# Optimization experiments

Hardware: AMD Instinct MI355X
Metric: run time of the kernel (lower is better)

## Reference

```python
import jax, jax.numpy as jnp
import numpy as np

WS = 8   # window_size
NH = 4   # num_heads
EPS = 1e-5

def _rel_pos_index(ws):
    # Static Swin relative-position index, computed with numpy (constant).
    coords = np.stack(np.meshgrid(np.arange(ws), np.arange(ws), indexing='ij'))  # [2,ws,ws]
    cf = coords.reshape(2, -1)                       # [2, N]
    rel = cf[:, :, None] - cf[:, None, :]            # [2, N, N]
    rel = rel.transpose(1, 2, 0).copy()              # [N, N, 2]
    rel[:, :, 0] += ws - 1
    rel[:, :, 1] += ws - 1
    rel[:, :, 0] *= 2 * ws - 1
    return jnp.asarray(rel.sum(-1))                  # [N, N] int

def setup_inputs() -> dict:
    key = jax.random.key(0)
    ks = jax.random.split(key, 4)
    B, C, H, W = 8, 64, 256, 256
    return {
        'x': jax.random.normal(ks[0], (B, C, H, W), jnp.float32),
        'norm_w': jnp.ones((C,), jnp.float32),
        'norm_b': jnp.zeros((C,), jnp.float32),
        'qkv_w': jax.random.normal(ks[1], (3 * C, C), jnp.float32) * 0.05,
        'proj_w': jax.random.normal(ks[2], (C, C), jnp.float32) * 0.05,
        'attn_scale': jnp.ones((1,), jnp.float32) * 0.2,
        'rpb_table': jax.random.normal(ks[3], ((2 * WS - 1) ** 2, NH), jnp.float32) * 0.02,
    }

def reference(x, norm_w, norm_b, qkv_w, proj_w, attn_scale, rpb_table):
    B, C, H, W = x.shape
    ws, nh = WS, NH
    hd = C // nh
    N = ws * ws
    nwh, nww = H // ws, W // ws  # H,W multiples of ws -> pad branch is a no-op
    # window partition: [B,C,H,W] -> [B*nwh*nww, N, C]
    xw = x.reshape(B, C, nwh, ws, nww, ws).transpose(0, 2, 4, 3, 5, 1).reshape(-1, N, C)
    # LayerNorm over channels
    mu = xw.mean(-1, keepdims=True)
    var = xw.var(-1, keepdims=True)
    xn = (xw - mu) / jnp.sqrt(var + EPS) * norm_w + norm_b
    # qkv projection (torch Linear: y = x @ W.T), split heads
    qkv = (xn @ qkv_w.T).reshape(-1, N, 3, nh, hd).transpose(2, 0, 3, 1, 4)  # [3, Wn, h, N, hd]
    q, k, v = qkv[0], qkv[1], qkv[2]
    attn = jnp.einsum('whnd,whmd->whnm', q, k) * (hd ** -0.5)  # [Wn, h, N, N]
    # gathered relative position bias
    rpi = _rel_pos_index(ws)                      # [N, N]
    bias = rpb_table[rpi].transpose(2, 0, 1)      # [h, N, N]
    attn = jax.nn.softmax(attn + bias[None], axis=-1)
    out = jnp.einsum('whnm,whmd->whnd', attn, v)  # [Wn, h, N, hd]
    out = out.transpose(0, 2, 1, 3).reshape(-1, N, C)
    out = out @ proj_w.T
    # window reverse: -> [B, C, H, W]
    out = out.reshape(B, nwh, nww, ws, ws, C).transpose(0, 5, 1, 3, 2, 4).reshape(B, C, H, W)
    return x + attn_scale * out
```

## Files before the change

### kernel.cpp

```cpp
#include <hip/hip_runtime.h>
#include <hip/hip_bf16.h>

#define WSZ 8
#define NHE 4
#define CH 64

typedef unsigned short u16;
typedef __attribute__((ext_vector_type(8))) short short8;
typedef __attribute__((ext_vector_type(4))) short short4v;
typedef __attribute__((ext_vector_type(4))) float float4v;

__device__ __forceinline__ u16 f2bf(float f) {
    __hip_bfloat16 h = __float2bfloat16(f);
    return __builtin_bit_cast(u16, h);
}
__device__ __forceinline__ int SW(int row, int col) {
    return row * 64 + (col ^ ((row & 7) << 3));
}

#define MFMA(a, b, c) __builtin_amdgcn_mfma_f32_16x16x32_bf16(a, b, c, 0, 0, 0)
#define QKSC 0.36067376022224085f

__global__ void prep(const float* __restrict__ qkvw, const float* __restrict__ projw,
                     const float* __restrict__ rpb,
                     u16* __restrict__ wq, u16* __restrict__ wp, float* __restrict__ bl)
{
    int t = blockIdx.x * 256 + threadIdx.x;
    if (t < 12288) {
        int j = t & 7, nl = (t >> 3) & 15, q = (t >> 7) & 3, kt = (t >> 9) & 1, nt = t >> 10;
        wq[t] = f2bf(qkvw[(nt * 16 + nl) * CH + kt * 32 + q * 8 + j]);
    }
    if (t < 4096) {
        int j = t & 7, nl = (t >> 3) & 15, q = (t >> 7) & 3, kt = (t >> 9) & 1, wv = t >> 10;
        wp[t] = f2bf(projw[(wv * 16 + nl) * CH + kt * 32 + q * 8 + j]);
    }
    if (t < 16384) {
        int r = t & 3, nt = (t >> 2) & 3, lane = (t >> 4) & 63, mt = (t >> 10) & 3, h = t >> 12;
        int nl = lane & 15, q = lane >> 4;
        int tokm = mt * 16 + nl, tokn = nt * 16 + q * 4 + r;
        int im = tokm >> 3, jm = tokm & 7, in_ = tokn >> 3, jn = tokn & 7;
        bl[t] = rpb[((im - in_ + 7) * 15 + (jm - jn + 7)) * NHE + h] * 1.44269504088896341f;
    }
}

__global__ __launch_bounds__(256, 5) void win_attn(
    const float* __restrict__ x, const float* __restrict__ nw, const float* __restrict__ nb,
    const u16* __restrict__ wq, const u16* __restrict__ wp,
    const float* __restrict__ ascale, const float* __restrict__ biasl,
    float* __restrict__ out, int B, int H, int W)
{
    const int HWsz = H * W;
    const int nww = W / WSZ, nwh = H / WSZ;
    const int win = (blockIdx.x & 7) * ((int)gridDim.x >> 3) + (blockIdx.x >> 3);
    const int ww = win % nww;
    const int t1 = win / nww;
    const int wh = t1 % nwh;
    const int b  = t1 / nwh;

    const int tid  = threadIdx.x;
    const int lane = tid & 63;
    const int wv   = tid >> 6;
    const int q    = lane >> 4;
    const int nl   = lane & 15;

    __shared__ alignas(16) char smem[32768];
    u16*   XN  = (u16*)(smem);
    u16*   QW  = (u16*)(smem + 8192) + wv * 3072;
    u16*   KW  = QW + 1024;
    u16*   VW  = QW + 2048;
    float* PS  = (float*)(smem + 8192);
    float* PS2 = PS + 256;

    const int rowbase = (wh * WSZ) * W + ww * WSZ;
    const float* xw = x + (size_t)b * CH * HWsz + rowbase;
    const int tokoff = (lane >> 3) * W + (lane & 7);

    float xv[16];
    {
        const float* xc = xw + (size_t)(wv * 16) * HWsz + tokoff;
        #pragma unroll
        for (int ci = 0; ci < 16; ci++) xv[ci] = xc[(size_t)ci * HWsz];
        float s = 0.f, s2 = 0.f;
        #pragma unroll
        for (int ci = 0; ci < 16; ci++) { s += xv[ci]; s2 += xv[ci] * xv[ci]; }
        PS[wv * 64 + lane] = s;
        PS2[wv * 64 + lane] = s2;
    }
    __syncthreads();

    {
        float s  = PS[lane]  + PS[64 + lane]  + PS[128 + lane]  + PS[192 + lane];
        float s2 = PS2[lane] + PS2[64 + lane] + PS2[128 + lane] + PS2[192 + lane];
        float mu  = s * (1.f / 64.f);
        float var = s2 * (1.f / 64.f) - mu * mu;
        float rs  = rsqrtf(var + 1e-5f);
        float v[16];
        #pragma unroll
        for (int ci = 0; ci < 16; ci++) {
            int c = wv * 16 + ci;
            v[ci] = (xv[ci] - mu) * rs * nw[c] + nb[c];
        }
        #pragma unroll
        for (int g = 0; g < 2; g++) {
            short8 pk;
            #pragma unroll
            for (int j = 0; j < 8; j++) pk[j] = (short)f2bf(v[g * 8 + j]);
            *(short8*)&XN[lane * 64 + ((wv * 16 + g * 8) ^ ((lane & 7) << 3))] = pk;
        }
    }
    __syncthreads();

    short8 afr[4][2];
    #pragma unroll
    for (int mt = 0; mt < 4; mt++)
        #pragma unroll
        for (int kt = 0; kt < 2; kt++) {
            int m = mt * 16 + nl;
            int phys = (kt * 4 + q) ^ (m & 7);
            afr[mt][kt] = *(short8*)&XN[m * 64 + phys * 8];
        }
    short8 bfrs[3][2];
    #pragma unroll
    for (int nt3 = 0; nt3 < 3; nt3++) {
        int nt = wv + nt3 * 4;
        #pragma unroll
        for (int kt = 0; kt < 2; kt++)
            bfrs[nt3][kt] = *(const short8*)&wq[((((nt * 2 + kt) * 4 + q) * 16) + nl) * 8];
    }
    __syncthreads();

    #pragma unroll
    for (int nt3 = 0; nt3 < 3; nt3++) {
        #pragma unroll
        for (int mt = 0; mt < 4; mt++) {
            float4v acc = {0.f, 0.f, 0.f, 0.f};
            acc = MFMA(afr[mt][0], bfrs[nt3][0], acc);
            acc = MFMA(afr[mt][1], bfrs[nt3][1], acc);
            int tok0 = mt * 16 + q * 4;
            if (nt3 == 0) {
                #pragma unroll
                for (int r = 0; r < 4; r++) QW[(tok0 + r) * 16 + nl] = f2bf(acc[r]);
            } else if (nt3 == 1) {
                #pragma unroll
                for (int r = 0; r < 4; r++) KW[(tok0 + r) * 16 + nl] = f2bf(acc[r]);
            } else {
                short4v pk;
                pk[0] = (short)f2bf(acc[0]); pk[1] = (short)f2bf(acc[1]);
                pk[2] = (short)f2bf(acc[2]); pk[3] = (short)f2bf(acc[3]);
                int pt = tok0 ^ ((nl & 7) << 3);
                *(short4v*)&VW[nl * 64 + pt] = pk;
            }
        }
    }

    {
        const int h = wv;
        const short8 zero8 = {0, 0, 0, 0, 0, 0, 0, 0};
        short8 kfr[4], vfr[2];
        #pragma unroll
        for (int nt = 0; nt < 4; nt++)
            kfr[nt] = (q < 2) ? *(short8*)&KW[(nt * 16 + nl) * 16 + q * 8] : zero8;
        #pragma unroll
        for (int kt = 0; kt < 2; kt++) {
            int phys = (kt * 4 + q) ^ (nl & 7);
            vfr[kt] = *(short8*)&VW[nl * 64 + phys * 8];
        }
        u16* Pw = KW;
        #pragma unroll
        for (int mt = 0; mt < 4; mt++) {
            short8 qf = (q < 2) ? *(short8*)&QW[(mt * 16 + nl) * 16 + q * 8] : zero8;
            const float4v* bp = (const float4v*)(biasl + ((((h * 4 + mt) * 64) + lane) << 4));
            float4v sacc[4];
            #pragma unroll
            for (int nt = 0; nt < 4; nt++) {
                float4v z = {0.f, 0.f, 0.f, 0.f};
                sacc[nt] = MFMA(kfr[nt], qf, z);
            }
            float p[16], mx = -1e30f;
            #pragma unroll
            for (int nt = 0; nt < 4; nt++) {
                float4v blv = bp[nt];
                #pragma unroll
                for (int r = 0; r < 4; r++) {
                    float s = fmaf(sacc[nt][r], QKSC, blv[r]);
                    p[nt * 4 + r] = s;
                    mx = fmaxf(mx, s);
                }
            }
            mx = fmaxf(mx, __shfl_xor(mx, 16, 64));
            mx = fmaxf(mx, __shfl_xor(mx, 32, 64));
            float sum = 0.f;
            #pragma unroll
            for (int i = 0; i < 16; i++) {
                float e = __builtin_amdgcn_exp2f(p[i] - mx);
                p[i] = e;
                sum += e;
            }
            sum += __shfl_xor(sum, 16, 64);
            sum += __shfl_xor(sum, 32, 64);
            float inv = __builtin_amdgcn_rcpf(sum);
            #pragma unroll
            for (int nt = 0; nt < 4; nt++)
                #pragma unroll
                for (int r = 0; r < 4; r++)
                    Pw[SW(nl, nt * 16 + q * 4 + r)] = f2bf(p[nt * 4 + r] * inv);
            float4v oacc = {0.f, 0.f, 0.f, 0.f};
            #pragma unroll
            for (int kt = 0; kt < 2; kt++) {
                int phys = (kt * 4 + q) ^ (nl & 7);
                short8 pf = *(short8*)&Pw[nl * 64 + phys * 8];
                oacc = MFMA(pf, vfr[kt], oacc);
            }
            #pragma unroll
            for (int r = 0; r < 4; r++)
                XN[SW(mt * 16 + q * 4 + r, h * 16 + nl)] = f2bf(oacc[r]);
        }
    }
    __syncthreads();

    {
        const float asc = ascale[0];
        const int ch = wv * 16 + nl;
        const float* xrp = xw + (size_t)ch * HWsz;
        float4v xr[4];
        #pragma unroll
        for (int mt = 0; mt < 4; mt++) {
            int tok0 = mt * 16 + q * 4;
            xr[mt] = *(const float4v*)(xrp + (tok0 >> 3) * W + (tok0 & 7));
        }
        short8 wfr[2];
        #pragma unroll
        for (int kt = 0; kt < 2; kt++)
            wfr[kt] = *(const short8*)&wp[((((wv * 2 + kt) * 4 + q) * 16) + nl) * 8];
        float* outp = out + ((size_t)b * CH + ch) * HWsz + rowbase;
        #pragma unroll
        for (int mt = 0; mt < 4; mt++) {
            float4v yacc = {0.f, 0.f, 0.f, 0.f};
            #pragma unroll
            for (int kt = 0; kt < 2; kt++) {
                int m = mt * 16 + nl;
                int phys = (kt * 4 + q) ^ (m & 7);
                short8 of = *(short8*)&XN[m * 64 + phys * 8];
                yacc = MFMA(of, wfr[kt], yacc);
            }
            int tok0 = mt * 16 + q * 4;
            int i = tok0 >> 3, j = tok0 & 7;
            float4v y;
            y[0] = xr[mt][0] + asc * yacc[0];
            y[1] = xr[mt][1] + asc * yacc[1];
            y[2] = xr[mt][2] + asc * yacc[2];
            y[3] = xr[mt][3] + asc * yacc[3];
            *(float4v*)(outp + i * W + j) = y;
        }
    }
}

extern "C" void kernel_launch(void* const* d_in, const int* in_sizes, int n_in,
                              void* d_out, int out_size, void* d_ws, size_t ws_size,
                              hipStream_t stream) {
    const float* x     = (const float*)d_in[0];
    const float* nw    = (const float*)d_in[1];
    const float* nb    = (const float*)d_in[2];
    const float* qkvw  = (const float*)d_in[3];
    const float* projw = (const float*)d_in[4];
    const float* asc   = (const float*)d_in[5];
    const float* rpb   = (const float*)d_in[6];

    const int H = 256, W = 256;
    const int B = in_sizes[0] / (CH * H * W);
    const int nwin = B * (H / WSZ) * (W / WSZ);

    u16*   wq = (u16*)d_ws;
    u16*   wp = (u16*)((char*)d_ws + 24576);
    float* bl = (float*)((char*)d_ws + 32768);

    prep<<<64, 256, 0, stream>>>(qkvw, projw, rpb, wq, wp, bl);
    win_attn<<<nwin, 256, 0, stream>>>(x, nw, nb, wq, wp, asc, bl,
                                       (float*)d_out, B, H, W);
}
```

Baseline: 330.2 us.

## Gather relative position bias in-kernel from LDS table instead of precomputed global layout

Stops precomputing the expanded 16K-float bias array in the prep kernel. Each block instead loads the small 225x4 rpb table into shared memory, gathers its head's 64x64 bias into 16 float4 registers, and uses them in the softmax. This cuts per-block global bias reads from 64KB to about 3.6KB, at the cost of 64 more registers per thread, so launch bounds drop from 5 to 4 blocks per CU.

New measurement: 371.9 us. +12.6%, slower.

```diff
diff --git a/kernel.cpp b/kernel.cpp
--- a/kernel.cpp
+++ b/kernel.cpp
@@ -20,10 +20,10 @@
 
 #define MFMA(a, b, c) __builtin_amdgcn_mfma_f32_16x16x32_bf16(a, b, c, 0, 0, 0)
 #define QKSC 0.36067376022224085f
+#define LOG2E 1.44269504088896341f
 
 __global__ void prep(const float* __restrict__ qkvw, const float* __restrict__ projw,
-                     const float* __restrict__ rpb,
-                     u16* __restrict__ wq, u16* __restrict__ wp, float* __restrict__ bl)
+                     u16* __restrict__ wq, u16* __restrict__ wp)
 {
     int t = blockIdx.x * 256 + threadIdx.x;
     if (t < 12288) {
@@ -34,19 +34,12 @@
         int j = t & 7, nl = (t >> 3) & 15, q = (t >> 7) & 3, kt = (t >> 9) & 1, wv = t >> 10;
         wp[t] = f2bf(projw[(wv * 16 + nl) * CH + kt * 32 + q * 8 + j]);
     }
-    if (t < 16384) {
-        int r = t & 3, nt = (t >> 2) & 3, lane = (t >> 4) & 63, mt = (t >> 10) & 3, h = t >> 12;
-        int nl = lane & 15, q = lane >> 4;
-        int tokm = mt * 16 + nl, tokn = nt * 16 + q * 4 + r;
-        int im = tokm >> 3, jm = tokm & 7, in_ = tokn >> 3, jn = tokn & 7;
-        bl[t] = rpb[((im - in_ + 7) * 15 + (jm - jn + 7)) * NHE + h] * 1.44269504088896341f;
-    }
-}
-
-__global__ __launch_bounds__(256, 5) void win_attn(
+}
+
+__global__ __launch_bounds__(256, 4) void win_attn(
     const float* __restrict__ x, const float* __restrict__ nw, const float* __restrict__ nb,
     const u16* __restrict__ wq, const u16* __restrict__ wp,
-    const float* __restrict__ ascale, const float* __restrict__ biasl,
+    const float* __restrict__ ascale, const float* __restrict__ rpb,
     float* __restrict__ out, int B, int H, int W)
 {
     const int HWsz = H * W;
@@ -70,6 +63,7 @@
     u16*   VW  = QW + 2048;
     float* PS  = (float*)(smem + 8192);
     float* PS2 = PS + 256;
+    float* RPBL = (float*)(smem + 10752);
 
     const int rowbase = (wh * WSZ) * W + ww * WSZ;
     const float* xw = x + (size_t)b * CH * HWsz + rowbase;
@@ -80,6 +74,8 @@
         const float* xc = xw + (size_t)(wv * 16) * HWsz + tokoff;
         #pragma unroll
         for (int ci = 0; ci < 16; ci++) xv[ci] = xc[(size_t)ci * HWsz];
+        for (int e = tid; e < (2 * WSZ - 1) * (2 * WSZ - 1) * NHE; e += 256)
+            RPBL[e] = rpb[e] * LOG2E;
         float s = 0.f, s2 = 0.f;
         #pragma unroll
         for (int ci = 0; ci < 16; ci++) { s += xv[ci]; s2 += xv[ci] * xv[ci]; }
@@ -88,6 +84,7 @@
     }
     __syncthreads();
 
+    float4v biasr[16];
     {
         float s  = PS[lane]  + PS[64 + lane]  + PS[128 + lane]  + PS[192 + lane];
         float s2 = PS2[lane] + PS2[64 + lane] + PS2[128 + lane] + PS2[192 + lane];
@@ -106,6 +103,18 @@
             #pragma unroll
             for (int j = 0; j < 8; j++) pk[j] = (short)f2bf(v[g * 8 + j]);
             *(short8*)&XN[lane * 64 + ((wv * 16 + g * 8) ^ ((lane & 7) << 3))] = pk;
+        }
+        const int q2 = q >> 1, q14 = (q & 1) * 4, jm = nl & 7, imb = nl >> 3;
+        #pragma unroll
+        for (int mt = 0; mt < 4; mt++) {
+            int a = 15 * (mt * 2 + imb) + jm + 112;
+            #pragma unroll
+            for (int nt = 0; nt < 4; nt++) {
+                int bb = a - 15 * (nt * 2 + q2);
+                #pragma unroll
+                for (int r = 0; r < 4; r++)
+                    biasr[mt * 4 + nt][r] = RPBL[(bb - q14 - r) * NHE + wv];
+            }
         }
     }
     __syncthreads();
@@ -154,7 +163,6 @@
     }
 
     {
-        const int h = wv;
         const short8 zero8 = {0, 0, 0, 0, 0, 0, 0, 0};
         short8 kfr[4], vfr[2];
         #pragma unroll
@@ -169,7 +177,6 @@
         #pragma unroll
         for (int mt = 0; mt < 4; mt++) {
             short8 qf = (q < 2) ? *(short8*)&QW[(mt * 16 + nl) * 16 + q * 8] : zero8;
-            const float4v* bp = (const float4v*)(biasl + ((((h * 4 + mt) * 64) + lane) << 4));
             float4v sacc[4];
             #pragma unroll
             for (int nt = 0; nt < 4; nt++) {
@@ -179,7 +186,7 @@
             float p[16], mx = -1e30f;
             #pragma unroll
             for (int nt = 0; nt < 4; nt++) {
-                float4v blv = bp[nt];
+                float4v blv = biasr[mt * 4 + nt];
                 #pragma unroll
                 for (int r = 0; r < 4; r++) {
                     float s = fmaf(sacc[nt][r], QKSC, blv[r]);
@@ -213,7 +220,7 @@
             }
             #pragma unroll
             for (int r = 0; r < 4; r++)
-                XN[SW(mt * 16 + q * 4 + r, h * 16 + nl)] = f2bf(oacc[r]);
+                XN[SW(mt * 16 + q * 4 + r, wv * 16 + nl)] = f2bf(oacc[r]);
         }
     }
     __syncthreads();
@@ -270,11 +277,10 @@
     const int B = in_sizes[0] / (CH * H * W);
     const int nwin = B * (H / WSZ) * (W / WSZ);
 
-    u16*   wq = (u16*)d_ws;
-    u16*   wp = (u16*)((char*)d_ws + 24576);
-    float* bl = (float*)((char*)d_ws + 32768);
-
-    prep<<<64, 256, 0, stream>>>(qkvw, projw, rpb, wq, wp, bl);
-    win_attn<<<nwin, 256, 0, stream>>>(x, nw, nb, wq, wp, asc, bl,
+    u16* wq = (u16*)d_ws;
+    u16* wp = (u16*)((char*)d_ws + 24576);
+
+    prep<<<48, 256, 0, stream>>>(qkvw, projw, wq, wp);
+    win_attn<<<nwin, 256, 0, stream>>>(x, nw, nb, wq, wp, asc, rpb,
                                        (float*)d_out, B, H, W);
 }
```
